# Kernel optimization log

Measured on AMD Instinct MI355X. Metric: run time of the kernel, lower is better.

The kernel has to match this reference:

```python
import jax, jax.numpy as jnp
import numpy as np

V, D, NL, NC = 16, 256, 4, 2
MAXL, NSTATE, DCONV, EXPAND, HEADDIM = 1024, 64, 4, 2, 64
DIN = EXPAND * D            # 512 inner channels
H = DIN // HEADDIM          # 8 heads
P = HEADDIM                 # 64 head dim
CONV_DIM = DIN + 2 * NSTATE # 640 channels through depthwise conv
D_IN_PROJ = 2 * DIN + 2 * NSTATE + H  # 1160
B_, L_ = 2, 1024
EPS = 1e-5


def setup_inputs() -> dict:
    key = jax.random.key(0)
    ks = iter(jax.random.split(key, 32))

    def rn(shape, s=0.02):
        return jax.random.normal(next(ks), shape, jnp.float32) * s

    emb = rn((V, D)).at[4].set(0.0)  # padding_idx=4 row zeroed
    pos_emb = rn((MAXL, D))
    in_proj_w = rn((NL, D_IN_PROJ, D))
    conv_w = rn((NL, CONV_DIM, DCONV), 0.1)
    conv_b = rn((NL, CONV_DIM), 0.1)
    dt_bias = rn((NL, H), 0.5)
    A_log = jnp.log(jax.random.uniform(next(ks), (NL, H), jnp.float32, 1.0, 16.0))
    D_param = jnp.ones((NL, H), jnp.float32)
    norm_w = jnp.ones((NL, DIN), jnp.float32)
    out_proj_w = rn((NL, D, DIN))
    pooler_w = rn((D, D), 0.05)
    pooler_b = jnp.zeros((D,), jnp.float32)
    cls1_w = rn((D // 2, D), 0.05)
    cls1_b = jnp.zeros((D // 2,), jnp.float32)
    cls2_w = rn((NC, D // 2), 0.05)
    cls2_b = jnp.zeros((NC,), jnp.float32)
    input_ids = jax.random.randint(next(ks), (B_, L_), 0, V)
    return dict(input_ids=input_ids, emb=emb, pos_emb=pos_emb,
                in_proj_w=in_proj_w, conv_w=conv_w, conv_b=conv_b,
                dt_bias=dt_bias, A_log=A_log, D_param=D_param, norm_w=norm_w,
                out_proj_w=out_proj_w, pooler_w=pooler_w, pooler_b=pooler_b,
                cls1_w=cls1_w, cls1_b=cls1_b, cls2_w=cls2_w, cls2_b=cls2_b)


def _mamba2(x, Win, cw, cb, dtb, A_log, Dp, nw, Wout):
    Bsz, L, _ = x.shape
    zxbcdt = jnp.einsum('bld,pd->blp', x, Win)              # (B,L,2*DIN+2N+H)
    z = zxbcdt[..., :DIN]
    xBC = zxbcdt[..., DIN:DIN + CONV_DIM]
    dt = jax.nn.softplus(zxbcdt[..., -H:] + dtb)            # (B,L,H)
    # causal depthwise conv over time
    xBC = jnp.transpose(xBC, (0, 2, 1))                     # (B,C,L)
    xBC = jax.lax.conv_general_dilated(
        xBC, cw[:, None, :], (1,), [(DCONV - 1, 0)],
        dimension_numbers=('NCH', 'OIH', 'NCH'),
        feature_group_count=CONV_DIM)
    xBC = jax.nn.silu(jnp.transpose(xBC, (0, 2, 1)) + cb)   # (B,L,C)
    xs = xBC[..., :DIN].reshape(Bsz, L, H, P)
    Bm = xBC[..., DIN:DIN + NSTATE]                         # (B,L,N)
    Cm = xBC[..., DIN + NSTATE:]                            # (B,L,N)
    A = -jnp.exp(A_log)                                     # (H,)
    dA = jnp.exp(dt * A)                                    # (B,L,H)
    dBx = dt[..., None, None] * xs[..., None] * Bm[:, :, None, None, :]  # (B,L,H,P,N)

    def step(h, inp):
        dA_t, dBx_t, C_t = inp
        h = dA_t[:, :, None, None] * h + dBx_t              # (B,H,P,N)
        y = jnp.einsum('bhpn,bn->bhp', h, C_t)
        return h, y

    h0 = jnp.zeros((Bsz, H, P, NSTATE), x.dtype)
    _, y = jax.lax.scan(step, h0, (jnp.moveaxis(dA, 1, 0),
                                   jnp.moveaxis(dBx, 1, 0),
                                   jnp.moveaxis(Cm, 1, 0)))
    y = jnp.moveaxis(y, 0, 1) + Dp[None, None, :, None] * xs  # (B,L,H,P)
    y = y.reshape(Bsz, L, DIN) * jax.nn.silu(z)               # gated
    y = y * jax.lax.rsqrt(jnp.mean(y * y, axis=-1, keepdims=True) + EPS) * nw
    return jnp.einsum('bld,od->blo', y, Wout)


def reference(input_ids, emb, pos_emb, in_proj_w, conv_w, conv_b, dt_bias,
              A_log, D_param, norm_w, out_proj_w, pooler_w, pooler_b,
              cls1_w, cls1_b, cls2_w, cls2_b):
    L = input_ids.shape[1]
    x = emb[input_ids] + pos_emb[:L][None]                  # (B,L,D)
    for i in range(NL):
        x = x + _mamba2(x, in_proj_w[i], conv_w[i], conv_b[i], dt_bias[i],
                        A_log[i], D_param[i], norm_w[i], out_proj_w[i])
    pooled = (x.mean(axis=1) + x.max(axis=1)) * 0.5         # (B,D)
    pooled = jax.nn.gelu(pooled @ pooler_w.T + pooler_b, approximate=False)
    hcls = jax.nn.gelu(pooled @ cls1_w.T + cls1_b, approximate=False)
    return hcls @ cls2_w.T + cls2_b
```

## Files before the change

kernel.cpp:

```cpp
#include <hip/hip_runtime.h>
#include <math.h>

#define D_ 256
#define NL_ 4
#define NC_ 2
#define L_LEN 1024
#define NSTATE_ 64
#define DIN_ 512
#define H_ 8
#define P_ 64
#define CONVDIM_ 640
#define DPROJ_ 1160
#define EPS_ 1e-5f
#define NCH_ 16

typedef __attribute__((ext_vector_type(8))) short short8;
typedef __attribute__((ext_vector_type(4))) float f32x4;
typedef __attribute__((ext_vector_type(4))) unsigned short us4;

__device__ __forceinline__ float siluf(float x) { return x / (1.f + __expf(-x)); }
__device__ __forceinline__ float geluf(float x) { return 0.5f * x * (1.f + erff(x * 0.70710678118654752f)); }
__device__ __forceinline__ unsigned short f2bf(float f) {
    unsigned u = __float_as_uint(f);
    u += 0x7FFFu + ((u >> 16) & 1u);
    return (unsigned short)(u >> 16);
}
__device__ __forceinline__ float bf2f(unsigned short h) {
    return __uint_as_float(((unsigned)h) << 16);
}

__global__ void k_embed(const int* __restrict__ ids, const float* __restrict__ emb,
                        const float* __restrict__ pos, float* __restrict__ x,
                        unsigned short* __restrict__ xh, unsigned short* __restrict__ xl,
                        int total) {
    int i = blockIdx.x * blockDim.x + threadIdx.x;
    if (i >= total) return;
    int d = i & (D_ - 1);
    int bl = i >> 8;
    int l = bl & (L_LEN - 1);
    float v = emb[ids[bl] * D_ + d] + pos[l * D_ + d];
    x[i] = v;
    unsigned short h = f2bf(v);
    xh[i] = h;
    xl[i] = f2bf(v - bf2f(h));
}

__global__ void k_x2bf(const float* __restrict__ x, unsigned short* __restrict__ xh,
                       unsigned short* __restrict__ xl, int total4) {
    int i = blockIdx.x * blockDim.x + threadIdx.x;
    if (i >= total4) return;
    float4 f = ((const float4*)x)[i];
    unsigned short h0 = f2bf(f.x), h1 = f2bf(f.y), h2 = f2bf(f.z), h3 = f2bf(f.w);
    us4 hv = {h0, h1, h2, h3};
    us4 lv = {f2bf(f.x - bf2f(h0)), f2bf(f.y - bf2f(h1)),
              f2bf(f.z - bf2f(h2)), f2bf(f.w - bf2f(h3))};
    ((us4*)xh)[i] = hv;
    ((us4*)xl)[i] = lv;
}

__global__ void k_w2bf2(const float* __restrict__ Wi, const float* __restrict__ Wo,
                        const float* __restrict__ nw,
                        unsigned short* __restrict__ wih, unsigned short* __restrict__ wil,
                        unsigned short* __restrict__ woh, unsigned short* __restrict__ wol,
                        int nin, int ntot) {
    int i = blockIdx.x * blockDim.x + threadIdx.x;
    if (i >= ntot) return;
    if (i < nin) {
        float f = Wi[i];
        unsigned short h = f2bf(f);
        wih[i] = h;
        wil[i] = f2bf(f - bf2f(h));
    } else {
        int j = i - nin;
        int layer = j / (D_ * DIN_);
        int k = j % DIN_;
        float f = Wo[j] * nw[layer * DIN_ + k];
        unsigned short h = f2bf(f);
        woh[j] = h;
        wol[j] = f2bf(f - bf2f(h));
    }
}

__global__ void __launch_bounds__(256) gemm_in(const unsigned short* __restrict__ Ahg,
        const unsigned short* __restrict__ Alg,
        const unsigned short* __restrict__ Bhi, const unsigned short* __restrict__ Blo,
        float* __restrict__ C, int M, int N, int K) {
    __shared__ __align__(16) unsigned short Ah[64 * 72];
    __shared__ __align__(16) unsigned short Al[64 * 72];
    __shared__ __align__(16) unsigned short Bh[64 * 72];
    __shared__ __align__(16) unsigned short Bl[64 * 72];
    const int tid = threadIdx.x;
    const int col0 = blockIdx.x * 64;
    const int row0 = blockIdx.y * 64;

    const int sar = tid >> 2, sas = (tid & 3) * 16;
    const bool bok = (col0 + sar) < N;
    const unsigned short* ahptr = Ahg + (size_t)(row0 + sar) * K + sas;
    const unsigned short* alptr = Alg + (size_t)(row0 + sar) * K + sas;
    const unsigned short* bhptr = Bhi + (size_t)(col0 + sar) * K + sas;
    const unsigned short* blptr = Blo + (size_t)(col0 + sar) * K + sas;

    short8 pah0 = *(const short8*)ahptr, pah1 = *(const short8*)(ahptr + 8);
    short8 pal0 = *(const short8*)alptr, pal1 = *(const short8*)(alptr + 8);
    short8 pbh0 = {0,0,0,0,0,0,0,0}, pbh1 = {0,0,0,0,0,0,0,0};
    short8 pbl0 = {0,0,0,0,0,0,0,0}, pbl1 = {0,0,0,0,0,0,0,0};
    if (bok) {
        pbh0 = *(const short8*)bhptr; pbh1 = *(const short8*)(bhptr + 8);
        pbl0 = *(const short8*)blptr; pbl1 = *(const short8*)(blptr + 8);
    }

    const int wave = tid >> 6, lane = tid & 63;
    const int lq = lane >> 4, lm = lane & 15;
    f32x4 acc[4] = {};
    const int nsteps = K >> 6;
    for (int s = 0; s < nsteps; ++s) {
        __syncthreads();
        *(short8*)&Ah[sar * 72 + sas] = pah0;
        *(short8*)&Ah[sar * 72 + sas + 8] = pah1;
        *(short8*)&Al[sar * 72 + sas] = pal0;
        *(short8*)&Al[sar * 72 + sas + 8] = pal1;
        *(short8*)&Bh[sar * 72 + sas] = pbh0;
        *(short8*)&Bh[sar * 72 + sas + 8] = pbh1;
        *(short8*)&Bl[sar * 72 + sas] = pbl0;
        *(short8*)&Bl[sar * 72 + sas + 8] = pbl1;
        __syncthreads();
        if (s + 1 < nsteps) {
            int ko = (s + 1) * 64;
            pah0 = *(const short8*)(ahptr + ko); pah1 = *(const short8*)(ahptr + ko + 8);
            pal0 = *(const short8*)(alptr + ko); pal1 = *(const short8*)(alptr + ko + 8);
            if (bok) {
                pbh0 = *(const short8*)(bhptr + ko); pbh1 = *(const short8*)(bhptr + ko + 8);
                pbl0 = *(const short8*)(blptr + ko); pbl1 = *(const short8*)(blptr + ko + 8);
            }
        }
#pragma unroll
        for (int k32 = 0; k32 < 2; ++k32) {
            const int kof = k32 * 32 + lq * 8;
            short8 bh[4], bl[4];
#pragma unroll
            for (int ct = 0; ct < 4; ++ct) {
                bh[ct] = *(const short8*)&Bh[(ct * 16 + lm) * 72 + kof];
                bl[ct] = *(const short8*)&Bl[(ct * 16 + lm) * 72 + kof];
            }
            short8 ah = *(const short8*)&Ah[(wave * 16 + lm) * 72 + kof];
            short8 al = *(const short8*)&Al[(wave * 16 + lm) * 72 + kof];
#pragma unroll
            for (int ct = 0; ct < 4; ++ct) {
                acc[ct] = __builtin_amdgcn_mfma_f32_16x16x32_bf16(ah, bh[ct], acc[ct], 0, 0, 0);
                acc[ct] = __builtin_amdgcn_mfma_f32_16x16x32_bf16(ah, bl[ct], acc[ct], 0, 0, 0);
                acc[ct] = __builtin_amdgcn_mfma_f32_16x16x32_bf16(al, bh[ct], acc[ct], 0, 0, 0);
            }
        }
    }
#pragma unroll
    for (int ct = 0; ct < 4; ++ct) {
        int col = col0 + ct * 16 + lm;
        if (col >= N) continue;
        int rbase = row0 + wave * 16 + lq * 4;
#pragma unroll
        for (int reg = 0; reg < 4; ++reg) {
            C[(size_t)(rbase + reg) * N + col] = acc[ct][reg];
        }
    }
}

__global__ void __launch_bounds__(256) gemm_outs(const unsigned short* __restrict__ Ghg,
        const unsigned short* __restrict__ Glg, const float* __restrict__ rowssq,
        const unsigned short* __restrict__ Bhi, const unsigned short* __restrict__ Blo,
        float* __restrict__ x) {
    __shared__ __align__(16) unsigned short Ah[64 * 72];
    __shared__ __align__(16) unsigned short Al[64 * 72];
    __shared__ __align__(16) unsigned short Bh[64 * 72];
    __shared__ __align__(16) unsigned short Bl[64 * 72];
    const int tid = threadIdx.x;
    const int col0 = blockIdx.x * 64;
    const int row0 = blockIdx.y * 64;
    const int kbase = blockIdx.z * 128;
    const int sar = tid >> 2, sas = (tid & 3) * 16;
    const unsigned short* ahptr = Ghg + (size_t)(row0 + sar) * DIN_ + kbase + sas;
    const unsigned short* alptr = Glg + (size_t)(row0 + sar) * DIN_ + kbase + sas;
    const unsigned short* bhptr = Bhi + (size_t)(col0 + sar) * DIN_ + kbase + sas;
    const unsigned short* blptr = Blo + (size_t)(col0 + sar) * DIN_ + kbase + sas;

    short8 pah0 = *(const short8*)ahptr, pah1 = *(const short8*)(ahptr + 8);
    short8 pal0 = *(const short8*)alptr, pal1 = *(const short8*)(alptr + 8);
    short8 pbh0 = *(const short8*)bhptr, pbh1 = *(const short8*)(bhptr + 8);
    short8 pbl0 = *(const short8*)blptr, pbl1 = *(const short8*)(blptr + 8);

    const int wave = tid >> 6, lane = tid & 63;
    const int lq = lane >> 4, lm = lane & 15;
    f32x4 acc[4] = {};
    for (int s = 0; s < 2; ++s) {
        __syncthreads();
        *(short8*)&Ah[sar * 72 + sas] = pah0;
        *(short8*)&Ah[sar * 72 + sas + 8] = pah1;
        *(short8*)&Al[sar * 72 + sas] = pal0;
        *(short8*)&Al[sar * 72 + sas + 8] = pal1;
        *(short8*)&Bh[sar * 72 + sas] = pbh0;
        *(short8*)&Bh[sar * 72 + sas + 8] = pbh1;
        *(short8*)&Bl[sar * 72 + sas] = pbl0;
        *(short8*)&Bl[sar * 72 + sas + 8] = pbl1;
        __syncthreads();
        if (s + 1 < 2) {
            int ko = 64;
            pah0 = *(const short8*)(ahptr + ko); pah1 = *(const short8*)(ahptr + ko + 8);
            pal0 = *(const short8*)(alptr + ko); pal1 = *(const short8*)(alptr + ko + 8);
            pbh0 = *(const short8*)(bhptr + ko); pbh1 = *(const short8*)(bhptr + ko + 8);
            pbl0 = *(const short8*)(blptr + ko); pbl1 = *(const short8*)(blptr + ko + 8);
        }
#pragma unroll
        for (int k32 = 0; k32 < 2; ++k32) {
            const int kof = k32 * 32 + lq * 8;
            short8 bh[4], bl[4];
#pragma unroll
            for (int ct = 0; ct < 4; ++ct) {
                bh[ct] = *(const short8*)&Bh[(ct * 16 + lm) * 72 + kof];
                bl[ct] = *(const short8*)&Bl[(ct * 16 + lm) * 72 + kof];
            }
            short8 ah = *(const short8*)&Ah[(wave * 16 + lm) * 72 + kof];
            short8 al = *(const short8*)&Al[(wave * 16 + lm) * 72 + kof];
#pragma unroll
            for (int ct = 0; ct < 4; ++ct) {
                acc[ct] = __builtin_amdgcn_mfma_f32_16x16x32_bf16(ah, bh[ct], acc[ct], 0, 0, 0);
                acc[ct] = __builtin_amdgcn_mfma_f32_16x16x32_bf16(ah, bl[ct], acc[ct], 0, 0, 0);
                acc[ct] = __builtin_amdgcn_mfma_f32_16x16x32_bf16(al, bh[ct], acc[ct], 0, 0, 0);
            }
        }
    }
    {
        int rbase = row0 + wave * 16 + lq * 4;
        float sc[4];
#pragma unroll
        for (int reg = 0; reg < 4; ++reg)
            sc[reg] = rsqrtf(rowssq[rbase + reg] * (1.f / DIN_) + EPS_);
#pragma unroll
        for (int ct = 0; ct < 4; ++ct) {
            int col = col0 + ct * 16 + lm;
#pragma unroll
            for (int reg = 0; reg < 4; ++reg) {
                atomicAdd(&x[(size_t)(rbase + reg) * D_ + col], sc[reg] * acc[ct][reg]);
            }
        }
    }
}

__global__ void __launch_bounds__(512) k_ssmA(const float* __restrict__ zx,
        const float* __restrict__ cw, const float* __restrict__ cb,
        const float* __restrict__ dtbias, const float* __restrict__ Alog,
        const float* __restrict__ Dp,
        float* __restrict__ Sbuf, float* __restrict__ decay,
        float* __restrict__ Ctil, float* __restrict__ y, float* __restrict__ rowssq) {
    __shared__ float U[64][65];
    __shared__ float V[64][65];
    __shared__ float W[64][65];
    __shared__ float sdt[64], cs[64], wj[64];
    const int c = blockIdx.x, bh = blockIdx.y;
    const int b = bh >> 3, h = bh & 7;
    const int l0 = c << 6;
    const int tid = threadIdx.x, wid8 = tid >> 6, lane = tid & 63;

    if (h == 0 && tid < 64) rowssq[b * L_LEN + l0 + tid] = 0.f;

    const int chx = h * P_ + lane;
    const int chb = DIN_ + lane;
    const int chc = DIN_ + NSTATE_ + lane;
    float wx0 = cw[chx * 4], wx1 = cw[chx * 4 + 1], wx2 = cw[chx * 4 + 2], wx3 = cw[chx * 4 + 3];
    float wb0 = cw[chb * 4], wb1 = cw[chb * 4 + 1], wb2 = cw[chb * 4 + 2], wb3 = cw[chb * 4 + 3];
    float wc0 = cw[chc * 4], wc1 = cw[chc * 4 + 1], wc2 = cw[chc * 4 + 2], wc3 = cw[chc * 4 + 3];
    float bx = cb[chx], bb = cb[chb], bc = cb[chc];

    for (int r = 0; r < 64; r += 8) {
        int j = r + wid8;
        int l = l0 + j;
        float ax = bx, ab = bb, ac = bc;
#pragma unroll
        for (int k = 0; k < 4; ++k) {
            int t = l - 3 + k;
            if (t >= 0) {
                const float* row = zx + (size_t)(b * L_LEN + t) * DPROJ_;
                float wxk = (k == 0) ? wx0 : (k == 1) ? wx1 : (k == 2) ? wx2 : wx3;
                float wbk = (k == 0) ? wb0 : (k == 1) ? wb1 : (k == 2) ? wb2 : wb3;
                float wck = (k == 0) ? wc0 : (k == 1) ? wc1 : (k == 2) ? wc2 : wc3;
                ax += wxk * row[DIN_ + chx];
                ab += wbk * row[DIN_ + chb];
                ac += wck * row[DIN_ + chc];
            }
        }
        U[j][lane] = siluf(ax);
        V[j][lane] = siluf(ab);
        W[j][lane] = siluf(ac);
    }
    if (tid < 64) {
        float xv = zx[(size_t)(b * L_LEN + l0 + tid) * DPROJ_ + (DPROJ_ - H_) + h] + dtbias[h];
        float sp = fmaxf(xv, 0.f) + log1pf(__expf(-fabsf(xv)));
        sdt[tid] = sp;
        float v = sp * (-__expf(Alog[h]));
#pragma unroll
        for (int off = 1; off < 64; off <<= 1) {
            float t = __shfl_up(v, off, 64);
            if (tid >= off) v += t;
        }
        cs[tid] = v;
        float tot = __shfl(v, 63, 64);
        wj[tid] = __expf(tot - v) * sp;
        if (tid == 63) decay[bh * NCH_ + c] = __expf(tot);
    }
    __syncthreads();

    const int t4 = (tid & 15) * 4;
    const int r4 = ((tid >> 4) & 15) * 4;
    const size_t sbase = (size_t)(bh * NCH_ + c) * 4096;

    if (tid < 256) {
        float acc[4][4] = {};
        for (int j = 0; j < 64; ++j) {
            float w = wj[j];
            float4 xv = *(const float4*)&U[j][r4];
            float4 bv = *(const float4*)&V[j][t4];
            float xw[4] = {xv.x * w, xv.y * w, xv.z * w, xv.w * w};
#pragma unroll
            for (int ii = 0; ii < 4; ++ii) {
                acc[ii][0] += xw[ii] * bv.x;
                acc[ii][1] += xw[ii] * bv.y;
                acc[ii][2] += xw[ii] * bv.z;
                acc[ii][3] += xw[ii] * bv.w;
            }
        }
#pragma unroll
        for (int ii = 0; ii < 4; ++ii) {
            float4 v = {acc[ii][0], acc[ii][1], acc[ii][2], acc[ii][3]};
            *(float4*)&Sbuf[sbase + (size_t)(r4 + ii) * 64 + t4] = v;
        }
    }
    for (int r = 0; r < 64; r += 8) {
        int ii = r + wid8;
        Ctil[sbase + ii * 64 + lane] = __expf(cs[ii]) * W[ii][lane];
    }
    float wt[4][4];
    if (tid < 256) {
        float g[4][4] = {};
        for (int ng = 0; ng < 64; ng += 4) {
            float4 cf[4], bf[4];
#pragma unroll
            for (int ii = 0; ii < 4; ++ii) cf[ii] = *(const float4*)&W[r4 + ii][ng];
#pragma unroll
            for (int jj = 0; jj < 4; ++jj) bf[jj] = *(const float4*)&V[t4 + jj][ng];
#pragma unroll
            for (int ii = 0; ii < 4; ++ii)
#pragma unroll
                for (int jj = 0; jj < 4; ++jj)
                    g[ii][jj] += cf[ii].x * bf[jj].x + cf[ii].y * bf[jj].y +
                                 cf[ii].z * bf[jj].z + cf[ii].w * bf[jj].w;
        }
#pragma unroll
        for (int ii = 0; ii < 4; ++ii) {
            int i = r4 + ii;
            float csi = cs[i];
#pragma unroll
            for (int jj = 0; jj < 4; ++jj) {
                int j = t4 + jj;
                wt[ii][jj] = (j <= i) ? __expf(fminf(csi - cs[j], 0.f)) * sdt[j] * g[ii][jj] : 0.f;
            }
        }
    }
    __syncthreads();
    if (tid < 256) {
#pragma unroll
        for (int jj = 0; jj < 4; ++jj) {
            float4 v = {wt[0][jj], wt[1][jj], wt[2][jj], wt[3][jj]};
            *(float4*)&V[t4 + jj][r4] = v;
        }
    }
    __syncthreads();
    if (tid < 256) {
        float acc[4][4] = {};
        for (int j = 0; j < 64; ++j) {
            float4 wv = *(const float4*)&V[j][r4];
            float4 xv = *(const float4*)&U[j][t4];
            float ws[4] = {wv.x, wv.y, wv.z, wv.w};
#pragma unroll
            for (int ii = 0; ii < 4; ++ii) {
                acc[ii][0] += ws[ii] * xv.x;
                acc[ii][1] += ws[ii] * xv.y;
                acc[ii][2] += ws[ii] * xv.z;
                acc[ii][3] += ws[ii] * xv.w;
            }
        }
        float Dh = Dp[h];
#pragma unroll
        for (int ii = 0; ii < 4; ++ii) {
            float4 xv = *(const float4*)&U[r4 + ii][t4];
            float4 v = {acc[ii][0] + Dh * xv.x, acc[ii][1] + Dh * xv.y,
                        acc[ii][2] + Dh * xv.z, acc[ii][3] + Dh * xv.w};
            *(float4*)&y[(size_t)(b * L_LEN + l0 + r4 + ii) * DIN_ + h * P_ + t4] = v;
        }
    }
}

__global__ void __launch_bounds__(512) k_inter(const float* __restrict__ Sbuf,
        const float* __restrict__ Ctil, const float* __restrict__ decay,
        const float* __restrict__ zx, const float* __restrict__ y,
        unsigned short* __restrict__ gh, unsigned short* __restrict__ gl,
        float* __restrict__ rowssq) {
    __shared__ float Sm[64][65];
    __shared__ float Cm[64][65];
    const int c = blockIdx.x, bh = blockIdx.y;
    const int b = bh >> 3, h = bh & 7;
    const int l0 = c << 6;
    const int tid = threadIdx.x, wid8 = tid >> 6, lane = tid & 63;
    const size_t bhbase = (size_t)bh * NCH_ * 4096;

    float dec[NCH_];
#pragma unroll
    for (int k = 0; k < NCH_; ++k) dec[k] = decay[bh * NCH_ + k];

    float acc8[8] = {};
    float wgt = 1.f;
    for (int cp = c - 1; cp >= 0; --cp) {
        const float* src = Sbuf + bhbase + (size_t)cp * 4096;
#pragma unroll
        for (int i = 0; i < 8; ++i) acc8[i] += wgt * src[i * 512 + tid];
        wgt *= dec[cp];
    }
#pragma unroll
    for (int i = 0; i < 8; ++i) Sm[i * 8 + wid8][lane] = acc8[i];

    const size_t base = bhbase + (size_t)c * 4096;
    for (int r = 0; r < 64; r += 8) {
        int pp = r + wid8;
        Cm[pp][lane] = Ctil[base + pp * 64 + lane];
    }
    __syncthreads();
    const int t4 = (tid & 15) * 4;
    const int r4 = ((tid >> 4) & 15) * 4;
    if (tid < 256) {
        float acc[4][4] = {};
        if (c > 0) {
            for (int ng = 0; ng < 64; ng += 4) {
                float4 cf[4], sf[4];
#pragma unroll
                for (int ii = 0; ii < 4; ++ii) cf[ii] = *(const float4*)&Cm[r4 + ii][ng];
#pragma unroll
                for (int pp = 0; pp < 4; ++pp) sf[pp] = *(const float4*)&Sm[t4 + pp][ng];
#pragma unroll
                for (int ii = 0; ii < 4; ++ii)
#pragma unroll
                    for (int pp = 0; pp < 4; ++pp)
                        acc[ii][pp] += cf[ii].x * sf[pp].x + cf[ii].y * sf[pp].y +
                                       cf[ii].z * sf[pp].z + cf[ii].w * sf[pp].w;
            }
        }
        float ssq[4];
#pragma unroll
        for (int ii = 0; ii < 4; ++ii) {
            int row = b * L_LEN + l0 + r4 + ii;
            const float* yr = &y[(size_t)row * DIN_ + h * P_ + t4];
            const float* zr = &zx[(size_t)row * DPROJ_ + h * P_ + t4];
            float4 v = *(const float4*)yr;
            float4 z = *(const float4*)zr;
            v.x = (v.x + acc[ii][0]) * siluf(z.x);
            v.y = (v.y + acc[ii][1]) * siluf(z.y);
            v.z = (v.z + acc[ii][2]) * siluf(z.z);
            v.w = (v.w + acc[ii][3]) * siluf(z.w);
            unsigned short h0 = f2bf(v.x), h1 = f2bf(v.y), h2 = f2bf(v.z), h3 = f2bf(v.w);
            us4 hv = {h0, h1, h2, h3};
            us4 lv = {f2bf(v.x - bf2f(h0)), f2bf(v.y - bf2f(h1)),
                      f2bf(v.z - bf2f(h2)), f2bf(v.w - bf2f(h3))};
            *(us4*)&gh[(size_t)row * DIN_ + h * P_ + t4] = hv;
            *(us4*)&gl[(size_t)row * DIN_ + h * P_ + t4] = lv;
            ssq[ii] = v.x * v.x + v.y * v.y + v.z * v.z + v.w * v.w;
        }
#pragma unroll
        for (int o = 1; o < 16; o <<= 1) {
#pragma unroll
            for (int ii = 0; ii < 4; ++ii) ssq[ii] += __shfl_xor(ssq[ii], o, 64);
        }
        if ((tid & 15) == 0) {
#pragma unroll
            for (int ii = 0; ii < 4; ++ii)
                atomicAdd(&rowssq[b * L_LEN + l0 + r4 + ii], ssq[ii]);
        }
    }
}

__global__ void __launch_bounds__(256) k_pool1(const float* __restrict__ x,
        float* __restrict__ psum, float* __restrict__ pmax) {
    int s = blockIdx.x, b = blockIdx.y, t = threadIdx.x;
    const float* xb = x + ((size_t)b * L_LEN + s * 64) * D_ + t;
    float sm = 0.f, mx = -INFINITY;
    for (int l = 0; l < 64; l += 4) {
        float v0 = xb[(size_t)l * D_];
        float v1 = xb[(size_t)(l + 1) * D_];
        float v2 = xb[(size_t)(l + 2) * D_];
        float v3 = xb[(size_t)(l + 3) * D_];
        sm += v0 + v1 + v2 + v3;
        mx = fmaxf(mx, fmaxf(fmaxf(v0, v1), fmaxf(v2, v3)));
    }
    psum[(b * 16 + s) * 256 + t] = sm;
    pmax[(b * 16 + s) * 256 + t] = mx;
}

__global__ void __launch_bounds__(1024) k_pool2(const float* __restrict__ psum,
                           const float* __restrict__ pmax,
                           const float* __restrict__ pw, const float* __restrict__ pb,
                           const float* __restrict__ c1w, const float* __restrict__ c1b,
                           const float* __restrict__ c2w, const float* __restrict__ c2b,
                           float* __restrict__ out) {
    __shared__ float sp[256], s1[256], s2[128];
    int b = blockIdx.x, tid = threadIdx.x;
    if (tid < 256) {
        float ss = 0.f, mm = -INFINITY;
#pragma unroll
        for (int s = 0; s < 16; ++s) {
            ss += psum[(b * 16 + s) * 256 + tid];
            mm = fmaxf(mm, pmax[(b * 16 + s) * 256 + tid]);
        }
        sp[tid] = (ss * (1.f / L_LEN) + mm) * 0.5f;
    }
    __syncthreads();
    {
        int o = tid >> 2, part = tid & 3;
        const float* wrow = pw + (size_t)o * 256 + part * 64;
        const float* sv = sp + part * 64;
        float acc = 0.f;
        for (int d = 0; d < 64; d += 4) {
            float4 w4 = *(const float4*)(wrow + d);
            float4 x4 = *(const float4*)(sv + d);
            acc += w4.x * x4.x + w4.y * x4.y + w4.z * x4.z + w4.w * x4.w;
        }
        acc += __shfl_xor(acc, 1, 64);
        acc += __shfl_xor(acc, 2, 64);
        if (part == 0) s1[o] = geluf(acc + pb[o]);
    }
    __syncthreads();
    {
        int o = tid >> 3, part = tid & 7;
        const float* wrow = c1w + (size_t)o * 256 + part * 32;
        const float* sv = s1 + part * 32;
        float acc = 0.f;
        for (int d = 0; d < 32; d += 4) {
            float4 w4 = *(const float4*)(wrow + d);
            float4 x4 = *(const float4*)(sv + d);
            acc += w4.x * x4.x + w4.y * x4.y + w4.z * x4.z + w4.w * x4.w;
        }
        acc += __shfl_xor(acc, 1, 64);
        acc += __shfl_xor(acc, 2, 64);
        acc += __shfl_xor(acc, 4, 64);
        if (part == 0) s2[o] = geluf(acc + c1b[o]);
    }
    __syncthreads();
    if (tid < 2) {
        float a = c2b[tid];
        for (int d = 0; d < 128; ++d) a += s2[d] * c2w[tid * 128 + d];
        out[b * NC_ + tid] = a;
    }
}

extern "C" void kernel_launch(void* const* d_in, const int* in_sizes, int n_in,
                              void* d_out, int out_size, void* d_ws, size_t ws_size,
                              hipStream_t stream) {
    const int* ids    = (const int*)d_in[0];
    const float* emb  = (const float*)d_in[1];
    const float* pos  = (const float*)d_in[2];
    const float* Wins = (const float*)d_in[3];
    const float* cw   = (const float*)d_in[4];
    const float* cb   = (const float*)d_in[5];
    const float* dtb  = (const float*)d_in[6];
    const float* Alog = (const float*)d_in[7];
    const float* Dpar = (const float*)d_in[8];
    const float* nw   = (const float*)d_in[9];
    const float* Wout = (const float*)d_in[10];
    const float* pw   = (const float*)d_in[11];
    const float* pb   = (const float*)d_in[12];
    const float* c1w  = (const float*)d_in[13];
    const float* c1b  = (const float*)d_in[14];
    const float* c2w  = (const float*)d_in[15];
    const float* c2b  = (const float*)d_in[16];
    float* out = (float*)d_out;

    const int NWIN = NL_ * DPROJ_ * D_;
    const int NWOUT = NL_ * D_ * DIN_;
    const int NG = 1048576;
    const int NX = 524288;

    float* ws = (float*)d_ws;
    float* x      = ws;
    float* zx     = x + 524288;
    float* y      = zx + 2375680;
    float* Sbuf   = y + 1048576;
    float* Ctil   = Sbuf + 1048576;
    float* decay  = Ctil + 1048576;
    float* rowssq = decay + 256;
    unsigned short* winh = (unsigned short*)(rowssq + 2048);
    unsigned short* winl = winh + NWIN;
    unsigned short* woh  = winl + NWIN;
    unsigned short* wol  = woh + NWOUT;
    unsigned short* gh   = wol + NWOUT;
    unsigned short* gl   = gh + NG;
    unsigned short* xh   = gl + NG;
    unsigned short* xl   = xh + NX;
    float* psum = (float*)(xl + NX);
    float* pmax = psum + 2 * 16 * 256;

    k_w2bf2<<<(NWIN + NWOUT + 255) / 256, 256, 0, stream>>>(
        Wins, Wout, nw, winh, winl, woh, wol, NWIN, NWIN + NWOUT);
    k_embed<<<2048, 256, 0, stream>>>(ids, emb, pos, x, xh, xl, NX);
    for (int i = 0; i < NL_; ++i) {
        size_t wo_in = (size_t)i * DPROJ_ * D_;
        size_t wo_out = (size_t)i * D_ * DIN_;
        gemm_in<<<dim3(19, 32), 256, 0, stream>>>(
            xh, xl, winh + wo_in, winl + wo_in, zx, 2048, DPROJ_, D_);
        k_ssmA<<<dim3(NCH_, 16), 512, 0, stream>>>(
            zx, cw + (size_t)i * CONVDIM_ * 4, cb + (size_t)i * CONVDIM_,
            dtb + i * H_, Alog + i * H_, Dpar + i * H_, Sbuf, decay, Ctil, y, rowssq);
        k_inter<<<dim3(NCH_, 16), 512, 0, stream>>>(Sbuf, Ctil, decay, zx, y, gh, gl, rowssq);
        gemm_outs<<<dim3(4, 32, 4), 256, 0, stream>>>(
            gh, gl, rowssq, woh + wo_out, wol + wo_out, x);
        if (i + 1 < NL_) {
            k_x2bf<<<(NX / 4 + 255) / 256, 256, 0, stream>>>(x, xh, xl, NX / 4);
        }
    }
    k_pool1<<<dim3(16, 2), 256, 0, stream>>>(x, psum, pmax);
    k_pool2<<<2, 1024, 0, stream>>>(psum, pmax, pw, pb, c1w, c1b, c2w, c2b, out);
}
```

Measured before the change: 350.4 us.

## Merge prep kernels and fuse residual bf16 split into out-proj GEMM via last-block counters

Combines the weight-splitting and embedding kernels into one prep launch that also zeroes a counter array. The per-layer x-to-bf16 hi/lo conversion kernel is removed. Instead, the last split-K block of gemm_outs to finish each output tile, detected with an atomic counter and thread fences, converts that tile of x. This saves four kernel launches per forward pass, at the cost of extra fences and atomics plus a serial tail in whichever block finishes each tile last.

After: 446.0 us. +27.3%, slower.

```diff
diff --git a/kernel.cpp b/kernel.cpp
--- a/kernel.cpp
+++ b/kernel.cpp
@@ -29,48 +29,22 @@
     return __uint_as_float(((unsigned)h) << 16);
 }
 
-__global__ void k_embed(const int* __restrict__ ids, const float* __restrict__ emb,
-                        const float* __restrict__ pos, float* __restrict__ x,
-                        unsigned short* __restrict__ xh, unsigned short* __restrict__ xl,
-                        int total) {
+__global__ void k_prep(const float* __restrict__ Wi, const float* __restrict__ Wo,
+                       const float* __restrict__ nw,
+                       unsigned short* __restrict__ wih, unsigned short* __restrict__ wil,
+                       unsigned short* __restrict__ woh, unsigned short* __restrict__ wol,
+                       const int* __restrict__ ids, const float* __restrict__ emb,
+                       const float* __restrict__ pos, float* __restrict__ x,
+                       unsigned short* __restrict__ xh, unsigned short* __restrict__ xl,
+                       int* __restrict__ counters,
+                       int nin, int nout, int nemb) {
     int i = blockIdx.x * blockDim.x + threadIdx.x;
-    if (i >= total) return;
-    int d = i & (D_ - 1);
-    int bl = i >> 8;
-    int l = bl & (L_LEN - 1);
-    float v = emb[ids[bl] * D_ + d] + pos[l * D_ + d];
-    x[i] = v;
-    unsigned short h = f2bf(v);
-    xh[i] = h;
-    xl[i] = f2bf(v - bf2f(h));
-}
-
-__global__ void k_x2bf(const float* __restrict__ x, unsigned short* __restrict__ xh,
-                       unsigned short* __restrict__ xl, int total4) {
-    int i = blockIdx.x * blockDim.x + threadIdx.x;
-    if (i >= total4) return;
-    float4 f = ((const float4*)x)[i];
-    unsigned short h0 = f2bf(f.x), h1 = f2bf(f.y), h2 = f2bf(f.z), h3 = f2bf(f.w);
-    us4 hv = {h0, h1, h2, h3};
-    us4 lv = {f2bf(f.x - bf2f(h0)), f2bf(f.y - bf2f(h1)),
-              f2bf(f.z - bf2f(h2)), f2bf(f.w - bf2f(h3))};
-    ((us4*)xh)[i] = hv;
-    ((us4*)xl)[i] = lv;
-}
-
-__global__ void k_w2bf2(const float* __restrict__ Wi, const float* __restrict__ Wo,
-                        const float* __restrict__ nw,
-                        unsigned short* __restrict__ wih, unsigned short* __restrict__ wil,
-                        unsigned short* __restrict__ woh, unsigned short* __restrict__ wol,
-                        int nin, int ntot) {
-    int i = blockIdx.x * blockDim.x + threadIdx.x;
-    if (i >= ntot) return;
     if (i < nin) {
         float f = Wi[i];
         unsigned short h = f2bf(f);
         wih[i] = h;
         wil[i] = f2bf(f - bf2f(h));
-    } else {
+    } else if (i < nin + nout) {
         int j = i - nin;
         int layer = j / (D_ * DIN_);
         int k = j % DIN_;
@@ -78,6 +52,18 @@
         unsigned short h = f2bf(f);
         woh[j] = h;
         wol[j] = f2bf(f - bf2f(h));
+    } else if (i < nin + nout + nemb) {
+        int k = i - nin - nout;
+        int d = k & (D_ - 1);
+        int bl = k >> 8;
+        int l = bl & (L_LEN - 1);
+        float v = emb[ids[bl] * D_ + d] + pos[l * D_ + d];
+        x[k] = v;
+        unsigned short h = f2bf(v);
+        xh[k] = h;
+        xl[k] = f2bf(v - bf2f(h));
+    } else if (i < nin + nout + nemb + 128) {
+        counters[i - nin - nout - nemb] = 0;
     }
 }
 
@@ -167,11 +153,13 @@
 __global__ void __launch_bounds__(256) gemm_outs(const unsigned short* __restrict__ Ghg,
         const unsigned short* __restrict__ Glg, const float* __restrict__ rowssq,
         const unsigned short* __restrict__ Bhi, const unsigned short* __restrict__ Blo,
-        float* __restrict__ x) {
+        float* __restrict__ x, unsigned short* __restrict__ xh,
+        unsigned short* __restrict__ xl, int* __restrict__ counters, int emit) {
     __shared__ __align__(16) unsigned short Ah[64 * 72];
     __shared__ __align__(16) unsigned short Al[64 * 72];
     __shared__ __align__(16) unsigned short Bh[64 * 72];
     __shared__ __align__(16) unsigned short Bl[64 * 72];
+    __shared__ int lastflag;
     const int tid = threadIdx.x;
     const int col0 = blockIdx.x * 64;
     const int row0 = blockIdx.y * 64;
@@ -239,6 +227,29 @@
 #pragma unroll
             for (int reg = 0; reg < 4; ++reg) {
                 atomicAdd(&x[(size_t)(rbase + reg) * D_ + col], sc[reg] * acc[ct][reg]);
+            }
+        }
+    }
+    if (emit) {
+        __threadfence();
+        if (tid == 0) {
+            int old = atomicAdd(&counters[blockIdx.y * 4 + blockIdx.x], 1);
+            lastflag = (old == 3);
+        }
+        __syncthreads();
+        if (lastflag) {
+            if (tid == 0) counters[blockIdx.y * 4 + blockIdx.x] = 0;
+            __threadfence();
+            for (int e = tid; e < 64 * 16; e += 256) {
+                int r = e >> 4, c4 = (e & 15) * 4;
+                size_t idx = (size_t)(row0 + r) * D_ + col0 + c4;
+                float4 f = *(const float4*)&x[idx];
+                unsigned short h0 = f2bf(f.x), h1 = f2bf(f.y), h2 = f2bf(f.z), h3 = f2bf(f.w);
+                us4 hv = {h0, h1, h2, h3};
+                us4 lv = {f2bf(f.x - bf2f(h0)), f2bf(f.y - bf2f(h1)),
+                          f2bf(f.z - bf2f(h2)), f2bf(f.w - bf2f(h3))};
+                *(us4*)&xh[idx] = hv;
+                *(us4*)&xl[idx] = lv;
             }
         }
     }
@@ -601,10 +612,12 @@
     unsigned short* xl   = xh + NX;
     float* psum = (float*)(xl + NX);
     float* pmax = psum + 2 * 16 * 256;
-
-    k_w2bf2<<<(NWIN + NWOUT + 255) / 256, 256, 0, stream>>>(
-        Wins, Wout, nw, winh, winl, woh, wol, NWIN, NWIN + NWOUT);
-    k_embed<<<2048, 256, 0, stream>>>(ids, emb, pos, x, xh, xl, NX);
+    int* counters = (int*)(pmax + 2 * 16 * 256);
+
+    const int NPREP = NWIN + NWOUT + NX + 128;
+    k_prep<<<(NPREP + 255) / 256, 256, 0, stream>>>(
+        Wins, Wout, nw, winh, winl, woh, wol,
+        ids, emb, pos, x, xh, xl, counters, NWIN, NWOUT, NX);
     for (int i = 0; i < NL_; ++i) {
         size_t wo_in = (size_t)i * DPROJ_ * D_;
         size_t wo_out = (size_t)i * D_ * DIN_;
@@ -615,10 +628,8 @@
             dtb + i * H_, Alog + i * H_, Dpar + i * H_, Sbuf, decay, Ctil, y, rowssq);
         k_inter<<<dim3(NCH_, 16), 512, 0, stream>>>(Sbuf, Ctil, decay, zx, y, gh, gl, rowssq);
         gemm_outs<<<dim3(4, 32, 4), 256, 0, stream>>>(
-            gh, gl, rowssq, woh + wo_out, wol + wo_out, x);
-        if (i + 1 < NL_) {
-            k_x2bf<<<(NX / 4 + 255) / 256, 256, 0, stream>>>(x, xh, xl, NX / 4);
-        }
+            gh, gl, rowssq, woh + wo_out, wol + wo_out, x, xh, xl, counters,
+            (i + 1 < NL_) ? 1 : 0);
     }
     k_pool1<<<dim3(16, 2), 256, 0, stream>>>(x, psum, pmax);
     k_pool2<<<2, 1024, 0, stream>>>(psum, pmax, pw, pb, c1w, c1b, c2w, c2b, out);
```
